# Kernel tuning notes

Hardware: AMD Instinct MI355X
Metric: run time of the kernel (lower is better)

Reference implementation:

```python
import jax, jax.numpy as jnp
import numpy as np

KMAX = 192  # static upper bound on sampled subset size k (E[k]~116, std~10 for our vals)


def _dpp_sample(vals, vecs, seed):
    """Sequential DPP sampling (Hough et al. algorithm), jit-compatible via
    fixed-width column padding (KMAX) and lax.while_loop over the k iterations.
    The original's nested classical Gram-Schmidt re-orthonormalization is
    expressed as a QR factorization with the R-diagonal sign convention of GS."""
    n = vals.shape[0]
    key = jax.random.key(seed)
    k_idx, k_loop = jax.random.split(key)

    # Bernoulli selection of eigenvectors: rand(n) < vals/(vals+1)
    index = jax.random.uniform(k_idx, (n,)) < vals / (vals + 1.0)
    k = jnp.sum(index.astype(jnp.int32))
    kk = jnp.minimum(k, KMAX)

    # Pack selected eigenvector columns to the left (stable sort: True first)
    order = jnp.argsort(~index)
    colmask0 = (jnp.arange(KMAX) < kk).astype(vals.dtype)
    V0 = vecs[:, order[:KMAX]] * colmask0[None, :]  # [n, KMAX]

    cols = jnp.arange(KMAX)

    def cond(st):
        i, V, subset = st
        return i < kk

    def body(st):
        i, V, subset = st
        m = kk - i  # number of active columns
        # p_i = ||V[i,:]||^2 over active columns (inactive cols are zero)
        p = jnp.sum(V * V, axis=1)
        c = jnp.cumsum(p / jnp.sum(p))
        u = jax.random.uniform(jax.random.fold_in(k_loop, i))
        item = jnp.argmax(u < c)  # first index where cdf exceeds u
        subset = subset.at[item].set(jnp.asarray(1.0, subset.dtype))
        # first active column j with |V[item, j]| > 0
        jmask = (jnp.abs(V[item]) > 0) & (cols < m)
        j = jnp.argmax(jmask)
        Vj = V[:, j]
        # delete column j (shift left), shrink active width to m-1
        src = jnp.minimum(jnp.where(cols >= j, cols + 1, cols), KMAX - 1)
        newmask = (cols < (m - 1)).astype(V.dtype)
        Vd = V[:, src] * newmask[None, :]
        # eliminate: V <- V - Vj * V[item,:] / Vj[item]
        Ve = (Vd - jnp.outer(Vj, Vd[item] / Vj[item])) * newmask[None, :]
        # re-orthonormalize active columns (classical GS == QR with positive R diag)
        Q, R = jnp.linalg.qr(Ve)
        d = jnp.diagonal(R)
        Q = Q * jnp.where(d >= 0, 1.0, -1.0)[None, :]
        Vn = Q * newmask[None, :]
        Vn = jnp.where(m > 1, Vn, V)  # original skips update when V has 1 column
        return (i + 1, Vn, subset)

    subset0 = jnp.zeros((n,), vals.dtype)
    _, _, subset = jax.lax.while_loop(cond, body, (jnp.int32(0), V0, subset0))
    # original returns all-ones when every eigenvector is selected
    return jnp.where(k == n, jnp.ones((n,), vals.dtype), subset)


def setup_inputs() -> dict:
    key = jax.random.key(0)
    k1, k2 = jax.random.split(key)
    n = 2048
    # eigenvalues in (0.01, 0.11) so E[|subset|] ~ 0.054*n ~ 116 << KMAX
    e = jax.random.uniform(k1, (n,), jnp.float32) * 0.1 + 0.01
    # orthonormal eigenvectors (proper eigendecomposition of a DPP kernel)
    v = jnp.linalg.qr(jax.random.normal(k2, (n, n), jnp.float32))[0]
    return {"e": e, "v": v, "seed": 0}


def reference(e, v, seed):
    return _dpp_sample(e, v, seed)
```

## Files before the change

kernel.cpp:

```cpp
#include <hip/hip_runtime.h>
#include <hip/hip_fp16.h>
#include <stdint.h>
#include <stddef.h>

#define N 2048
#define KMX 192
#define NTH 1024

typedef _Float16 f16x2 __attribute__((ext_vector_type(2)));
typedef _Float16 f16x4 __attribute__((ext_vector_type(4)));

#if defined(__has_builtin)
#if __has_builtin(__builtin_amdgcn_fdot2)
#define HAS_FDOT2 1
#endif
#endif

__device__ __forceinline__ f16x2 bch2(unsigned u) { return __builtin_bit_cast(f16x2, u); }
__device__ __forceinline__ unsigned packh2(float a, float b) {
  unsigned ua = (unsigned)__half_as_ushort(__float2half(a));
  unsigned ub = (unsigned)__half_as_ushort(__float2half(b));
  return ua | (ub << 16);
}
__device__ __forceinline__ float dot2acc(unsigned c, unsigned y, float acc) {
#ifdef HAS_FDOT2
  return __builtin_amdgcn_fdot2(bch2(c), bch2(y), acc, false);
#else
  f16x2 cv = bch2(c), yv = bch2(y);
  acc = fmaf((float)cv[0], (float)yv[0], acc);
  acc = fmaf((float)cv[1], (float)yv[1], acc);
  return acc;
#endif
}

__device__ __forceinline__ void tfround(unsigned &x0, unsigned &x1, const int d) {
  x0 += x1;
  x1 = (x1 << d) | (x1 >> (32 - d));
  x1 ^= x0;
}

__device__ __forceinline__ uint2 tf2x32(unsigned k0, unsigned k1, unsigned c0, unsigned c1) {
  unsigned ks2 = k0 ^ k1 ^ 0x1BD11BDAu;
  unsigned x0 = c0 + k0, x1 = c1 + k1;
  tfround(x0,x1,13); tfround(x0,x1,15); tfround(x0,x1,26); tfround(x0,x1,6);
  x0 += k1;  x1 += ks2 + 1u;
  tfround(x0,x1,17); tfround(x0,x1,29); tfround(x0,x1,16); tfround(x0,x1,24);
  x0 += ks2; x1 += k0 + 2u;
  tfround(x0,x1,13); tfround(x0,x1,15); tfround(x0,x1,26); tfround(x0,x1,6);
  x0 += k0;  x1 += k1 + 3u;
  tfround(x0,x1,17); tfround(x0,x1,29); tfround(x0,x1,16); tfround(x0,x1,24);
  x0 += k1;  x1 += ks2 + 4u;
  tfround(x0,x1,13); tfround(x0,x1,15); tfround(x0,x1,26); tfround(x0,x1,6);
  x0 += ks2; x1 += k0 + 5u;
  uint2 r; r.x = x0; r.y = x1;
  return r;
}

__device__ __forceinline__ float u01(unsigned bits) {
  return __uint_as_float((bits >> 9) | 0x3f800000u) - 1.0f;
}

__global__ void k_select(const float* __restrict__ e, const int* __restrict__ seedp,
                         int* __restrict__ hdr, int* __restrict__ sel) {
  __shared__ unsigned kx0, kx1;
  __shared__ int cnt_s[256];
  __shared__ int pre_s[256];
  const int tid = threadIdx.x;
  if (tid == 0) {
    unsigned seed = (unsigned)seedp[0];
    uint2 kidx  = tf2x32(0u, seed, 0u, 0u);
    uint2 kloop = tf2x32(0u, seed, 0u, 1u);
    kx0 = kidx.x; kx1 = kidx.y;
    hdr[2] = (int)kloop.x;
    hdr[3] = (int)kloop.y;
  }
  __syncthreads();
  const unsigned a0 = kx0, a1 = kx1;
  int flags = 0;
  #pragma unroll
  for (int r = 0; r < 8; ++r) {
    const int i = tid * 8 + r;
    uint2 o = tf2x32(a0, a1, 0u, (unsigned)i);
    float u = u01(o.x ^ o.y);
    float ev = e[i];
    float thr = ev / (ev + 1.0f);
    if (u < thr) flags |= (1 << r);
  }
  cnt_s[tid] = __popc(flags);
  __syncthreads();
  if (tid == 0) {
    int acc = 0;
    for (int t2 = 0; t2 < 256; ++t2) { pre_s[t2] = acc; acc += cnt_s[t2]; }
    hdr[1] = acc;
    hdr[0] = acc < KMX ? acc : KMX;
  }
  __syncthreads();
  int off = pre_s[tid];
  #pragma unroll
  for (int r = 0; r < 8; ++r) {
    if (flags & (1 << r)) {
      if (off < KMX) sel[off] = tid * 8 + r;
      ++off;
    }
  }
}

__global__ void k_gather(const float* __restrict__ v, const int* __restrict__ hdr,
                         const int* __restrict__ sel, float* __restrict__ G,
                         __half* __restrict__ Gh) {
  const int j = blockIdx.y;
  const int i = blockIdx.x * 256 + threadIdx.x;
  float val = 0.f;
  if (j < hdr[0]) val = v[(size_t)i * N + sel[j]];
  G[j * N + i] = val;
  Gh[j * N + i] = __float2half(val);
}

__global__ void __launch_bounds__(256)
k_gram(const __half* __restrict__ Gh, const int* __restrict__ hdr,
       __half* __restrict__ Kh) {
  __shared__ __align__(16) __half As[32][64];
  __shared__ __align__(16) __half Bs[32][64];
  const int tid = threadIdx.x;
  const int i0 = blockIdx.y * 64;
  const int i1 = blockIdx.x * 64;
  const int tr = tid & 15, tc = tid >> 4;
  const int kk = hdr[0];
  int kc = (kk + 31) & ~31;
  if (kc > KMX) kc = KMX;

  float acc[4][4];
  #pragma unroll
  for (int r = 0; r < 4; ++r)
    #pragma unroll
    for (int c = 0; c < 4; ++c) acc[r][c] = 0.f;

  const int jr = tid >> 3, c8 = (tid & 7) * 8;
  for (int j0 = 0; j0 < kc; j0 += 32) {
    *(uint4*)&As[jr][c8] = *(const uint4*)(Gh + (size_t)(j0 + jr) * N + i0 + c8);
    *(uint4*)&Bs[jr][c8] = *(const uint4*)(Gh + (size_t)(j0 + jr) * N + i1 + c8);
    __syncthreads();
    #pragma unroll 8
    for (int k = 0; k < 32; ++k) {
      f16x4 a4 = *(const f16x4*)&As[k][tr * 4];
      f16x4 b4 = *(const f16x4*)&Bs[k][tc * 4];
      #pragma unroll
      for (int r = 0; r < 4; ++r)
        #pragma unroll
        for (int c = 0; c < 4; ++c)
          acc[r][c] = fmaf((float)a4[r], (float)b4[c], acc[r][c]);
    }
    __syncthreads();
  }
  #pragma unroll
  for (int r = 0; r < 4; ++r) {
    const int row = i0 + tr * 4 + r;
    uint2 w;
    w.x = packh2(acc[r][0], acc[r][1]);
    w.y = packh2(acc[r][2], acc[r][3]);
    *(uint2*)(Kh + (size_t)row * N + i1 + tc * 4) = w;
  }
}

__global__ void __launch_bounds__(NTH)
k_dpp_chol(const int* __restrict__ hdr, const __half* __restrict__ Kh,
           unsigned* __restrict__ YP, float* __restrict__ out) {
  __shared__ float p_s[N];
  __shared__ unsigned cpack_s[KMX / 2];
  __shared__ float u_s[KMX];
  __shared__ float wsum_s[16];
  __shared__ float rinv_sh;
  __shared__ int item_sh;

  const int tid  = threadIdx.x;
  const int lane = tid & 63;
  const int wave = tid >> 6;
  const int kk    = hdr[0];
  const int kfull = hdr[1];
  const unsigned kl0 = (unsigned)hdr[2];
  const unsigned kl1 = (unsigned)hdr[3];

  const float fill = (kfull == N) ? 1.0f : 0.0f;
  out[tid] = fill;
  out[tid + NTH] = fill;
  if (kfull == N || kk == 0) return;

  {
    const int i0 = 2 * tid;
    p_s[i0]     = (float)Kh[(size_t)i0 * N + i0];
    p_s[i0 + 1] = (float)Kh[(size_t)(i0 + 1) * N + i0 + 1];
    if (tid < KMX) {
      uint2 fk = tf2x32(kl0, kl1, 0u, (unsigned)tid);
      uint2 ob = tf2x32(fk.x, fk.y, 0u, 0u);
      u_s[tid] = u01(ob.x ^ ob.y);
    }
    if (tid == 0) item_sh = N;
  }
  __syncthreads();

  for (int t = 0; t < kk; ++t) {
    float a  = p_s[2 * tid];
    float b  = p_s[2 * tid + 1];
    float ts = a + b;
    float ws = ts;
    #pragma unroll
    for (int d = 1; d < 64; d <<= 1) {
      float o = __shfl_up(ws, d, 64);
      if (lane >= d) ws += o;
    }
    if (lane == 63) wsum_s[wave] = ws;
    __syncthreads();
    float S = 0.f, base_wave = 0.f;
    #pragma unroll
    for (int w = 0; w < 16; ++w) {
      float wv = wsum_s[w];
      if (w < wave) base_wave += wv;
      S += wv;
    }
    const float u = u_s[t];
    float excl = __shfl_up(ws, 1, 64);
    if (lane == 0) excl = 0.f;
    const float base = base_wave + excl;
    const float c0 = (base + a) / S;
    const float c1 = (base + ts) / S;
    const bool m0 = (u < c0);
    const bool m1 = (u < c1);
    unsigned long long bal = __ballot(m0 || m1);
    if (bal) {
      int first = (int)__builtin_ctzll(bal);
      if (lane == first) atomicMin(&item_sh, m0 ? 2 * tid : 2 * tid + 1);
    }
    __syncthreads();
    int item = item_sh;
    if (item >= N) item = 0;
    if (tid == 0) out[item] = 1.0f;
    if (t == kk - 1) break;

    if (tid < KMX / 2) {
      unsigned cu = 0;
      if (2 * tid < t) cu = YP[(size_t)tid * N + item] ^ 0x80008000u;
      cpack_s[tid] = cu;
    }
    if (tid == 0) {
      rinv_sh = 1.0f / sqrtf(fmaxf(p_s[item], 1e-30f));
      item_sh = N;
    }
    __syncthreads();

    {
      const float rinv = rinv_sh;
      const int npair = (t + 1) >> 1;
      unsigned kp = *(const unsigned*)(Kh + (size_t)item * N + 2 * tid);
      f16x2 kv = bch2(kp);
      float acc0 = (float)kv[0], acc1 = (float)kv[1];
      for (int sp = 0; sp < npair; ++sp) {
        unsigned cs = cpack_s[sp];
        uint2 yv = *(const uint2*)(YP + (size_t)sp * N + 2 * tid);
        acc0 = dot2acc(cs, yv.x, acc0);
        acc1 = dot2acc(cs, yv.y, acc1);
      }
      float y0 = acc0 * rinv, y1 = acc1 * rinv;
      p_s[2 * tid]     = fmaxf(p_s[2 * tid]     - y0 * y0, 0.f);
      p_s[2 * tid + 1] = fmaxf(p_s[2 * tid + 1] - y1 * y1, 0.f);
      const int spt = t >> 1;
      if ((t & 1) == 0) {
        uint2 w;
        w.x = packh2(y0, 0.f);
        w.y = packh2(y1, 0.f);
        *(uint2*)(YP + (size_t)spt * N + 2 * tid) = w;
      } else {
        unsigned short* Ys = (unsigned short*)YP;
        Ys[((size_t)spt * N + 2 * tid) * 2 + 1]     = __half_as_ushort(__float2half(y0));
        Ys[((size_t)spt * N + 2 * tid + 1) * 2 + 1] = __half_as_ushort(__float2half(y1));
      }
    }
  }
}

__global__ void __launch_bounds__(NTH)
k_dpp_main(const int* __restrict__ hdr, const float* __restrict__ G,
           const __half* __restrict__ Gh, float* __restrict__ D,
           float* __restrict__ out) {
  __shared__ float p_s[N];
  __shared__ float g_s[KMX];
  __shared__ float part[16 * KMX];
  __shared__ float u_s[KMX];
  __shared__ float wsum_s[16];
  __shared__ int item_sh;

  const int tid  = threadIdx.x;
  const int lane = tid & 63;
  const int wave = tid >> 6;
  const int kk    = hdr[0];
  const int kfull = hdr[1];
  const unsigned kl0 = (unsigned)hdr[2];
  const unsigned kl1 = (unsigned)hdr[3];

  const float fill = (kfull == N) ? 1.0f : 0.0f;
  out[tid] = fill;
  out[tid + NTH] = fill;
  if (kfull == N || kk == 0) return;

  const int kkr = (kk + 15) & ~15;

  {
    float s0a = 0.f, s0b = 0.f, s1a = 0.f, s1b = 0.f;
    const __half* base = Gh + 2 * tid;
    for (int j = 0; j < kkr; j += 4) {
      float2 f0 = __half22float2(*(const __half2*)(base + (j + 0) * N));
      float2 f1 = __half22float2(*(const __half2*)(base + (j + 1) * N));
      float2 f2 = __half22float2(*(const __half2*)(base + (j + 2) * N));
      float2 f3 = __half22float2(*(const __half2*)(base + (j + 3) * N));
      s0a = fmaf(f0.x, f0.x, s0a); s1a = fmaf(f0.y, f0.y, s1a);
      s0b = fmaf(f1.x, f1.x, s0b); s1b = fmaf(f1.y, f1.y, s1b);
      s0a = fmaf(f2.x, f2.x, s0a); s1a = fmaf(f2.y, f2.y, s1a);
      s0b = fmaf(f3.x, f3.x, s0b); s1b = fmaf(f3.y, f3.y, s1b);
    }
    p_s[2 * tid]     = s0a + s0b;
    p_s[2 * tid + 1] = s1a + s1b;
    if (tid < KMX) {
      uint2 fk = tf2x32(kl0, kl1, 0u, (unsigned)tid);
      uint2 ob = tf2x32(fk.x, fk.y, 0u, 0u);
      u_s[tid] = u01(ob.x ^ ob.y);
    }
    if (tid == 0) item_sh = N;
  }
  __syncthreads();

  for (int t = 0; t < kk; ++t) {
    float a  = p_s[2 * tid];
    float b  = p_s[2 * tid + 1];
    float ts = a + b;
    float ws = ts;
    #pragma unroll
    for (int d = 1; d < 64; d <<= 1) {
      float o = __shfl_up(ws, d, 64);
      if (lane >= d) ws += o;
    }
    if (lane == 63) wsum_s[wave] = ws;
    __syncthreads();
    float S = 0.f, base_wave = 0.f;
    #pragma unroll
    for (int w = 0; w < 16; ++w) {
      float wv = wsum_s[w];
      if (w < wave) base_wave += wv;
      S += wv;
    }
    const float u = u_s[t];
    float excl = __shfl_up(ws, 1, 64);
    if (lane == 0) excl = 0.f;
    const float base = base_wave + excl;
    const float c0 = (base + a) / S;
    const float c1 = (base + ts) / S;
    const bool m0 = (u < c0);
    const bool m1 = (u < c1);
    unsigned long long bal = __ballot(m0 || m1);
    if (bal) {
      int first = (int)__builtin_ctzll(bal);
      if (lane == first) atomicMin(&item_sh, m0 ? 2 * tid : 2 * tid + 1);
    }
    __syncthreads();
    int item = item_sh;
    if (item >= N) item = 0;
    if (tid == 0) out[item] = 1.0f;
    if (t == kk - 1) break;

    if (tid < KMX) g_s[tid] = G[tid * N + item];
    __syncthreads();

    {
      float g0 = g_s[lane], g1 = g_s[lane + 64], g2 = g_s[lane + 128];
      float a0 = 0.f, a1 = 0.f, a2 = 0.f;
      for (int s = wave; s < t; s += 16) {
        const float* Dr = D + s * KMX;
        float d0 = Dr[lane], d1 = Dr[lane + 64], d2 = Dr[lane + 128];
        float acc = fmaf(d0, g0, fmaf(d1, g1, d2 * g2));
        #pragma unroll
        for (int m = 1; m < 64; m <<= 1) acc += __shfl_xor(acc, m, 64);
        a0 = fmaf(acc, d0, a0); a1 = fmaf(acc, d1, a1); a2 = fmaf(acc, d2, a2);
      }
      part[wave * KMX + lane]       = a0;
      part[wave * KMX + lane + 64]  = a1;
      part[wave * KMX + lane + 128] = a2;
    }
    __syncthreads();
    if (tid < KMX) {
      float gg = g_s[tid];
      #pragma unroll
      for (int w = 0; w < 16; ++w) gg -= part[w * KMX + tid];
      g_s[tid] = gg;
    }
    __syncthreads();

    float gg2 = 0.f;
    {
      float g0 = g_s[lane], g1 = g_s[lane + 64], g2 = g_s[lane + 128];
      float a0 = 0.f, a1 = 0.f, a2 = 0.f;
      for (int s = wave; s < t; s += 16) {
        const float* Dr = D + s * KMX;
        float d0 = Dr[lane], d1 = Dr[lane + 64], d2 = Dr[lane + 128];
        float acc = fmaf(d0, g0, fmaf(d1, g1, d2 * g2));
        #pragma unroll
        for (int m = 1; m < 64; m <<= 1) acc += __shfl_xor(acc, m, 64);
        a0 = fmaf(acc, d0, a0); a1 = fmaf(acc, d1, a1); a2 = fmaf(acc, d2, a2);
      }
      part[wave * KMX + lane]       = a0;
      part[wave * KMX + lane + 64]  = a1;
      part[wave * KMX + lane + 128] = a2;
    }
    __syncthreads();
    if (tid < KMX) {
      float gg = g_s[tid];
      #pragma unroll
      for (int w = 0; w < 16; ++w) gg -= part[w * KMX + tid];
      gg2 = gg;
    }
    if (wave < 3) {
      float r = gg2 * gg2;
      #pragma unroll
      for (int m = 1; m < 64; m <<= 1) r += __shfl_xor(r, m, 64);
      if (lane == 0) wsum_s[wave] = r;
    }
    __syncthreads();
    const float rho = sqrtf(wsum_s[0] + wsum_s[1] + wsum_s[2]);
    if (tid < KMX) {
      float dj = gg2 / rho;
      g_s[tid] = dj;
      D[t * KMX + tid] = dj;
    }
    if (tid == 0) item_sh = N;
    __syncthreads();

    {
      float s0a = 0.f, s0b = 0.f, s1a = 0.f, s1b = 0.f;
      const __half* base2 = Gh + 2 * tid;
      for (int j = 0; j < kkr; j += 4) {
        float d0 = g_s[j], d1 = g_s[j + 1], d2 = g_s[j + 2], d3 = g_s[j + 3];
        float2 f0 = __half22float2(*(const __half2*)(base2 + (j + 0) * N));
        float2 f1 = __half22float2(*(const __half2*)(base2 + (j + 1) * N));
        float2 f2 = __half22float2(*(const __half2*)(base2 + (j + 2) * N));
        float2 f3 = __half22float2(*(const __half2*)(base2 + (j + 3) * N));
        s0a = fmaf(f0.x, d0, s0a); s1a = fmaf(f0.y, d0, s1a);
        s0b = fmaf(f1.x, d1, s0b); s1b = fmaf(f1.y, d1, s1b);
        s0a = fmaf(f2.x, d2, s0a); s1a = fmaf(f2.y, d2, s1a);
        s0b = fmaf(f3.x, d3, s0b); s1b = fmaf(f3.y, d3, s1b);
      }
      float s0 = s0a + s0b, s1 = s1a + s1b;
      p_s[2 * tid]     = fmaxf(p_s[2 * tid]     - s0 * s0, 0.f);
      p_s[2 * tid + 1] = fmaxf(p_s[2 * tid + 1] - s1 * s1, 0.f);
    }
  }
}

extern "C" void kernel_launch(void* const* d_in, const int* in_sizes, int n_in,
                              void* d_out, int out_size, void* d_ws, size_t ws_size,
                              hipStream_t stream) {
  (void)in_sizes; (void)n_in; (void)out_size;
  const float* e    = (const float*)d_in[0];
  const float* v    = (const float*)d_in[1];
  const int*   seed = (const int*)d_in[2];
  float* out = (float*)d_out;

  int* hdr = (int*)d_ws;
  int* sel = hdr + 8;

  if (ws_size >= (size_t)12 * 1024 * 1024) {
    __half*   Gh = (__half*)((char*)d_ws + 4096);
    float*    G  = (float*)((char*)d_ws + (size_t)1024 * 1024);
    unsigned* YP = (unsigned*)((char*)d_ws + (size_t)2560 * 1024);
    __half*   Kh = (__half*)((char*)d_ws + (size_t)4096 * 1024);

    k_select<<<1, 256, 0, stream>>>(e, seed, hdr, sel);
    k_gather<<<dim3(8, KMX), 256, 0, stream>>>(v, hdr, sel, G, Gh);
    k_gram<<<dim3(32, 32), 256, 0, stream>>>(Gh, hdr, Kh);
    k_dpp_chol<<<1, NTH, 0, stream>>>(hdr, Kh, YP, out);
  } else {
    float*  D  = (float*)((char*)d_ws + 1024);
    float*  G  = (float*)((char*)d_ws + (size_t)256 * 1024);
    __half* Gh = (__half*)((char*)d_ws + (size_t)2048 * 1024);

    k_select<<<1, 256, 0, stream>>>(e, seed, hdr, sel);
    k_gather<<<dim3(8, KMX), 256, 0, stream>>>(v, hdr, sel, G, Gh);
    k_dpp_main<<<1, NTH, 0, stream>>>(hdr, G, Gh, D, out);
  }
}
```

Before: 72.20 us.

## Pack Cholesky factor rows in fours and drop unused fp32 gather output

```diff
diff --git a/kernel.cpp b/kernel.cpp
--- a/kernel.cpp
+++ b/kernel.cpp
@@ -105,6 +105,15 @@
   }
 }
 
+__global__ void k_gather_h(const float* __restrict__ v, const int* __restrict__ hdr,
+                           const int* __restrict__ sel, __half* __restrict__ Gh) {
+  const int j = blockIdx.y;
+  const int i = blockIdx.x * 256 + threadIdx.x;
+  float val = 0.f;
+  if (j < hdr[0]) val = v[(size_t)i * N + sel[j]];
+  Gh[j * N + i] = __float2half(val);
+}
+
 __global__ void k_gather(const float* __restrict__ v, const int* __restrict__ hdr,
                          const int* __restrict__ sel, float* __restrict__ G,
                          __half* __restrict__ Gh) {
@@ -164,9 +173,9 @@
 
 __global__ void __launch_bounds__(NTH)
 k_dpp_chol(const int* __restrict__ hdr, const __half* __restrict__ Kh,
-           unsigned* __restrict__ YP, float* __restrict__ out) {
+           uint2* __restrict__ YQ, float* __restrict__ out) {
   __shared__ float p_s[N];
-  __shared__ unsigned cpack_s[KMX / 2];
+  __shared__ uint2 cpack_s[KMX / 4];
   __shared__ float u_s[KMX];
   __shared__ float wsum_s[16];
   __shared__ float rinv_sh;
@@ -217,12 +226,13 @@
       if (w < wave) base_wave += wv;
       S += wv;
     }
+    const float Sinv = 1.0f / S;
     const float u = u_s[t];
     float excl = __shfl_up(ws, 1, 64);
     if (lane == 0) excl = 0.f;
     const float base = base_wave + excl;
-    const float c0 = (base + a) / S;
-    const float c1 = (base + ts) / S;
+    const float c0 = (base + a) * Sinv;
+    const float c1 = (base + ts) * Sinv;
     const bool m0 = (u < c0);
     const bool m1 = (u < c1);
     unsigned long long bal = __ballot(m0 || m1);
@@ -236,9 +246,16 @@
     if (tid == 0) out[item] = 1.0f;
     if (t == kk - 1) break;
 
-    if (tid < KMX / 2) {
-      unsigned cu = 0;
-      if (2 * tid < t) cu = YP[(size_t)tid * N + item] ^ 0x80008000u;
+    if (tid * 4 < t) {
+      uint2 cu = YQ[(size_t)tid * N + item];
+      cu.x ^= 0x80008000u;
+      cu.y ^= 0x80008000u;
+      const int rem = t - 4 * tid;
+      if (rem < 4) {
+        if (rem == 1)      { cu.x &= 0x0000FFFFu; cu.y = 0u; }
+        else if (rem == 2) { cu.y = 0u; }
+        else               { cu.y &= 0x0000FFFFu; }
+      }
       cpack_s[tid] = cu;
     }
     if (tid == 0) {
@@ -249,30 +266,27 @@
 
     {
       const float rinv = rinv_sh;
-      const int npair = (t + 1) >> 1;
+      const int nq = (t + 3) >> 2;
       unsigned kp = *(const unsigned*)(Kh + (size_t)item * N + 2 * tid);
       f16x2 kv = bch2(kp);
       float acc0 = (float)kv[0], acc1 = (float)kv[1];
-      for (int sp = 0; sp < npair; ++sp) {
-        unsigned cs = cpack_s[sp];
-        uint2 yv = *(const uint2*)(YP + (size_t)sp * N + 2 * tid);
-        acc0 = dot2acc(cs, yv.x, acc0);
-        acc1 = dot2acc(cs, yv.y, acc1);
+      const uint2* Yp = YQ + 2 * tid;
+      #pragma unroll 2
+      for (int q = 0; q < nq; ++q) {
+        uint2 cs = cpack_s[q];
+        uint4 yv = *(const uint4*)(Yp + (size_t)q * N);
+        acc0 = dot2acc(cs.x, yv.x, acc0);
+        acc0 = dot2acc(cs.y, yv.y, acc0);
+        acc1 = dot2acc(cs.x, yv.z, acc1);
+        acc1 = dot2acc(cs.y, yv.w, acc1);
       }
       float y0 = acc0 * rinv, y1 = acc1 * rinv;
       p_s[2 * tid]     = fmaxf(p_s[2 * tid]     - y0 * y0, 0.f);
       p_s[2 * tid + 1] = fmaxf(p_s[2 * tid + 1] - y1 * y1, 0.f);
-      const int spt = t >> 1;
-      if ((t & 1) == 0) {
-        uint2 w;
-        w.x = packh2(y0, 0.f);
-        w.y = packh2(y1, 0.f);
-        *(uint2*)(YP + (size_t)spt * N + 2 * tid) = w;
-      } else {
-        unsigned short* Ys = (unsigned short*)YP;
-        Ys[((size_t)spt * N + 2 * tid) * 2 + 1]     = __half_as_ushort(__float2half(y0));
-        Ys[((size_t)spt * N + 2 * tid + 1) * 2 + 1] = __half_as_ushort(__float2half(y1));
-      }
+      unsigned short* Ys = (unsigned short*)YQ;
+      const size_t eb = ((size_t)(t >> 2) * N + 2 * tid) * 4;
+      Ys[eb + (t & 3)]     = __half_as_ushort(__float2half(y0));
+      Ys[eb + 4 + (t & 3)] = __half_as_ushort(__float2half(y1));
     }
   }
 }
@@ -465,15 +479,14 @@
   int* sel = hdr + 8;
 
   if (ws_size >= (size_t)12 * 1024 * 1024) {
-    __half*   Gh = (__half*)((char*)d_ws + 4096);
-    float*    G  = (float*)((char*)d_ws + (size_t)1024 * 1024);
-    unsigned* YP = (unsigned*)((char*)d_ws + (size_t)2560 * 1024);
-    __half*   Kh = (__half*)((char*)d_ws + (size_t)4096 * 1024);
+    __half* Gh = (__half*)((char*)d_ws + 4096);
+    uint2*  YQ = (uint2*)((char*)d_ws + (size_t)2560 * 1024);
+    __half* Kh = (__half*)((char*)d_ws + (size_t)4096 * 1024);
 
     k_select<<<1, 256, 0, stream>>>(e, seed, hdr, sel);
-    k_gather<<<dim3(8, KMX), 256, 0, stream>>>(v, hdr, sel, G, Gh);
+    k_gather_h<<<dim3(8, KMX), 256, 0, stream>>>(v, hdr, sel, Gh);
     k_gram<<<dim3(32, 32), 256, 0, stream>>>(Gh, hdr, Kh);
-    k_dpp_chol<<<1, NTH, 0, stream>>>(hdr, Kh, YP, out);
+    k_dpp_chol<<<1, NTH, 0, stream>>>(hdr, Kh, YQ, out);
   } else {
     float*  D  = (float*)((char*)d_ws + 1024);
     float*  G  = (float*)((char*)d_ws + (size_t)256 * 1024);
```

Result: faster. 65.75 us (-8.9%).
